# Optimization experiments

Hardware: AMD Instinct MI355X
Metric: run time of the kernel (lower is better)

The kernel has to match this reference:

```python
import jax, jax.numpy as jnp
import numpy as np

TOP_K = 2


def setup_inputs() -> dict:
    key = jax.random.key(0)
    k1, k2, k3, k4, k5 = jax.random.split(key, 5)
    T, H, I, E = 1024, 1024, 2816, 8
    return {
        "hidden_states": jax.random.normal(k1, (T, H), dtype=jnp.float32),
        "router_logits": jax.random.normal(k2, (T, E), dtype=jnp.float32),
        "w1": jax.random.normal(k3, (E, I, H), dtype=jnp.float32) * 0.02,
        "w3": jax.random.normal(k4, (E, I, H), dtype=jnp.float32) * 0.02,
        "w2": jax.random.normal(k5, (E, H, I), dtype=jnp.float32) * 0.02,
    }


def _gate_weights(router_logits):
    # top-k softmax with renormalization (Mixtral-style routing)
    probs = jax.nn.softmax(router_logits, axis=-1)          # [T, E]
    vals, idx = jax.lax.top_k(probs, TOP_K)                  # [T, K]
    vals = vals / jnp.sum(vals, axis=-1, keepdims=True)
    E = router_logits.shape[-1]
    # dense per-expert gate [T, E]: scatter top-k weights via one-hot
    onehot = jax.nn.one_hot(idx, E, dtype=vals.dtype)        # [T, K, E]
    return jnp.einsum("tk,tke->te", vals, onehot)


def reference(hidden_states, router_logits, w1, w3, w2):
    x = hidden_states.reshape(-1, hidden_states.shape[-1])   # [T, H]
    gate = _gate_weights(router_logits)                      # [T, E]
    # GatedMLP per expert: silu(x @ w1^T) * (x @ w3^T) @ w2^T
    h1 = jnp.einsum("th,eih->tei", x, w1)                    # [T, E, I]
    h3 = jnp.einsum("th,eih->tei", x, w3)
    act = jax.nn.silu(h1) * h3                               # [T, E, I]
    y = jnp.einsum("tei,ehi->teh", act, w2)                  # [T, E, H]
    out = jnp.einsum("teh,te->th", y, gate)                  # weighted combine
    return out
```

## Files before the change

kernel.cpp:

```cpp
#include <hip/hip_runtime.h>
#include <stdint.h>

#define T_TOK 1024
#define H_DIM 1024
#define I_DIM 2816
#define E_NUM 8

typedef __attribute__((ext_vector_type(8))) short bf16x8;
typedef __attribute__((ext_vector_type(4))) float f32x4;

struct Meta { int counts[E_NUM]; int tiles[E_NUM]; int offs[E_NUM]; };

__device__ __forceinline__ unsigned short f2b(float f) {
    unsigned u = __float_as_uint(f);
    u += 0x7fffu + ((u >> 16) & 1u);
    return (unsigned short)(u >> 16);
}

__global__ void route_kernel(const float* __restrict__ logits,
                             int* __restrict__ tok, float* __restrict__ gate,
                             Meta* __restrict__ meta) {
    __shared__ int cnt[E_NUM];
    const int tid = threadIdx.x;
    if (tid < E_NUM) cnt[tid] = 0;
    for (int j = tid; j < E_NUM * T_TOK; j += 1024) { tok[j] = 0; gate[j] = 0.f; }
    __syncthreads();

    float p[E_NUM];
    const float* lrow = logits + tid * E_NUM;
    float m = -1e30f;
    #pragma unroll
    for (int e = 0; e < E_NUM; ++e) { p[e] = lrow[e]; m = fmaxf(m, p[e]); }
    #pragma unroll
    for (int e = 0; e < E_NUM; ++e) p[e] = __expf(p[e] - m);
    int e0 = 0; float v0 = p[0];
    #pragma unroll
    for (int e = 1; e < E_NUM; ++e) if (p[e] > v0) { v0 = p[e]; e0 = e; }
    int e1 = -1; float v1 = -1.f;
    #pragma unroll
    for (int e = 0; e < E_NUM; ++e) if (e != e0 && p[e] > v1) { v1 = p[e]; e1 = e; }
    const float inv = 1.f / (v0 + v1);
    const float g0 = v0 * inv, g1 = v1 * inv;

    const int p0 = atomicAdd(&cnt[e0], 1);
    const int p1 = atomicAdd(&cnt[e1], 1);
    tok[e0 * T_TOK + p0] = tid; gate[e0 * T_TOK + p0] = g0;
    tok[e1 * T_TOK + p1] = tid; gate[e1 * T_TOK + p1] = g1;
    __syncthreads();
    if (tid == 0) {
        int off = 0;
        for (int e = 0; e < E_NUM; ++e) {
            const int c = cnt[e];
            const int t = (c + 127) >> 7;
            meta->counts[e] = c; meta->tiles[e] = t; meta->offs[e] = off;
            off += t * 128;
        }
    }
}

__global__ void cvt_x_kernel(const float* __restrict__ x, unsigned short* __restrict__ xb) {
    const int i = blockIdx.x * blockDim.x + threadIdx.x;
    const float4 v = ((const float4*)x)[i];
    ushort4 o; o.x = f2b(v.x); o.y = f2b(v.y); o.z = f2b(v.z); o.w = f2b(v.w);
    ((ushort4*)xb)[i] = o;
}

__launch_bounds__(256)
__global__ void gemm1_kernel(const unsigned short* __restrict__ xb,
                             const float* __restrict__ w1,
                             const float* __restrict__ w3,
                             const int* __restrict__ tok,
                             const Meta* __restrict__ meta,
                             unsigned short* __restrict__ act) {
    const int e = blockIdx.y;
    const int mt = blockIdx.z;
    if (mt >= meta->tiles[e]) return;
    const int it = blockIdx.x;
    const int tid = threadIdx.x;

    __shared__ __align__(16) unsigned short As[128 * 32];
    __shared__ __align__(16) unsigned short B1s[64 * 32];
    __shared__ __align__(16) unsigned short B3s[64 * 32];

    const int arow = tid >> 2, asub = tid & 3;
    const int t0 = tok[e * T_TOK + mt * 128 + arow];
    const int t1 = tok[e * T_TOK + mt * 128 + 64 + arow];
    const unsigned short* ap0 = xb + (size_t)t0 * H_DIM + asub * 8;
    const unsigned short* ap1 = xb + (size_t)t1 * H_DIM + asub * 8;
    unsigned short* al0 = &As[arow * 32 + asub * 8];
    unsigned short* al1 = &As[(64 + arow) * 32 + asub * 8];

    const int brow = tid >> 3, bsub = tid & 7;
    const size_t wbase = (size_t)e * I_DIM * H_DIM + (size_t)(it * 64) * H_DIM;
    const float* b1p0 = w1 + wbase + (size_t)brow * H_DIM + bsub * 4;
    const float* b1p1 = w1 + wbase + (size_t)(32 + brow) * H_DIM + bsub * 4;
    const float* b3p0 = w3 + wbase + (size_t)brow * H_DIM + bsub * 4;
    const float* b3p1 = w3 + wbase + (size_t)(32 + brow) * H_DIM + bsub * 4;
    unsigned short* bl10 = &B1s[brow * 32 + bsub * 4];
    unsigned short* bl11 = &B1s[(32 + brow) * 32 + bsub * 4];
    unsigned short* bl30 = &B3s[brow * 32 + bsub * 4];
    unsigned short* bl31 = &B3s[(32 + brow) * 32 + bsub * 4];

    const int wave = tid >> 6, lane = tid & 63;
    const int quad = lane >> 4, l15 = lane & 15;
    const int mbase = (wave >> 1) * 64;
    const int nbase = (wave & 1) * 32;

    f32x4 acc1[4][2], acc3[4][2];
    #pragma unroll
    for (int mi = 0; mi < 4; ++mi)
        #pragma unroll
        for (int ni = 0; ni < 2; ++ni) {
            acc1[mi][ni] = (f32x4){0.f, 0.f, 0.f, 0.f};
            acc3[mi][ni] = (f32x4){0.f, 0.f, 0.f, 0.f};
        }

    uint4 ra0 = *(const uint4*)(ap0), ra1 = *(const uint4*)(ap1);
    float4 r10 = *(const float4*)(b1p0), r11 = *(const float4*)(b1p1);
    float4 r30 = *(const float4*)(b3p0), r31 = *(const float4*)(b3p1);

    const int NK = H_DIM / 32;
    for (int ks = 0; ks < NK; ++ks) {
        __syncthreads();
        *(uint4*)al0 = ra0;
        *(uint4*)al1 = ra1;
        ushort4 c;
        c.x = f2b(r10.x); c.y = f2b(r10.y); c.z = f2b(r10.z); c.w = f2b(r10.w); *(ushort4*)bl10 = c;
        c.x = f2b(r11.x); c.y = f2b(r11.y); c.z = f2b(r11.z); c.w = f2b(r11.w); *(ushort4*)bl11 = c;
        c.x = f2b(r30.x); c.y = f2b(r30.y); c.z = f2b(r30.z); c.w = f2b(r30.w); *(ushort4*)bl30 = c;
        c.x = f2b(r31.x); c.y = f2b(r31.y); c.z = f2b(r31.z); c.w = f2b(r31.w); *(ushort4*)bl31 = c;
        __syncthreads();
        if (ks + 1 < NK) {
            const int k0 = (ks + 1) * 32;
            ra0 = *(const uint4*)(ap0 + k0);  ra1 = *(const uint4*)(ap1 + k0);
            r10 = *(const float4*)(b1p0 + k0); r11 = *(const float4*)(b1p1 + k0);
            r30 = *(const float4*)(b3p0 + k0); r31 = *(const float4*)(b3p1 + k0);
        }
        bf16x8 a[4];
        #pragma unroll
        for (int mi = 0; mi < 4; ++mi)
            a[mi] = *(const bf16x8*)&As[(mbase + mi * 16 + l15) * 32 + quad * 8];
        bf16x8 b1f[2], b3f[2];
        #pragma unroll
        for (int ni = 0; ni < 2; ++ni) {
            b1f[ni] = *(const bf16x8*)&B1s[(nbase + ni * 16 + l15) * 32 + quad * 8];
            b3f[ni] = *(const bf16x8*)&B3s[(nbase + ni * 16 + l15) * 32 + quad * 8];
        }
        #pragma unroll
        for (int mi = 0; mi < 4; ++mi)
            #pragma unroll
            for (int ni = 0; ni < 2; ++ni) {
                acc1[mi][ni] = __builtin_amdgcn_mfma_f32_16x16x32_bf16(a[mi], b1f[ni], acc1[mi][ni], 0, 0, 0);
                acc3[mi][ni] = __builtin_amdgcn_mfma_f32_16x16x32_bf16(a[mi], b3f[ni], acc3[mi][ni], 0, 0, 0);
            }
    }

    const int opad = meta->offs[e];
    #pragma unroll
    for (int mi = 0; mi < 4; ++mi)
        #pragma unroll
        for (int ni = 0; ni < 2; ++ni)
            #pragma unroll
            for (int rr = 0; rr < 4; ++rr) {
                const float v1 = acc1[mi][ni][rr];
                const float v3 = acc3[mi][ni][rr];
                const float s = v1 / (1.f + __expf(-v1)) * v3;
                const int row = opad + mt * 128 + mbase + mi * 16 + quad * 4 + rr;
                const int col = it * 64 + nbase + ni * 16 + l15;
                act[(size_t)row * I_DIM + col] = f2b(s);
            }
}

__launch_bounds__(256)
__global__ void gemm2_kernel(const unsigned short* __restrict__ act,
                             const float* __restrict__ w2,
                             const int* __restrict__ tok,
                             const float* __restrict__ gate,
                             const Meta* __restrict__ meta,
                             float* __restrict__ out) {
    const int e = blockIdx.y;
    const int mt = blockIdx.z;
    if (mt >= meta->tiles[e]) return;
    const int it = blockIdx.x;
    const int tid = threadIdx.x;
    const int opad = meta->offs[e];

    __shared__ __align__(16) unsigned short As[128 * 32];
    __shared__ __align__(16) unsigned short Bs[64 * 32];

    const int arow = tid >> 2, asub = tid & 3;
    const unsigned short* ap0 = act + (size_t)(opad + mt * 128 + arow) * I_DIM + asub * 8;
    const unsigned short* ap1 = act + (size_t)(opad + mt * 128 + 64 + arow) * I_DIM + asub * 8;
    unsigned short* al0 = &As[arow * 32 + asub * 8];
    unsigned short* al1 = &As[(64 + arow) * 32 + asub * 8];

    const int brow = tid >> 3, bsub = tid & 7;
    const size_t wbase = (size_t)e * H_DIM * I_DIM + (size_t)(it * 64) * I_DIM;
    const float* bp0 = w2 + wbase + (size_t)brow * I_DIM + bsub * 4;
    const float* bp1 = w2 + wbase + (size_t)(32 + brow) * I_DIM + bsub * 4;
    unsigned short* bl0 = &Bs[brow * 32 + bsub * 4];
    unsigned short* bl1 = &Bs[(32 + brow) * 32 + bsub * 4];

    const int wave = tid >> 6, lane = tid & 63;
    const int quad = lane >> 4, l15 = lane & 15;
    const int mbase = (wave >> 1) * 64;
    const int nbase = (wave & 1) * 32;

    f32x4 acc[4][2];
    #pragma unroll
    for (int mi = 0; mi < 4; ++mi)
        #pragma unroll
        for (int ni = 0; ni < 2; ++ni) acc[mi][ni] = (f32x4){0.f, 0.f, 0.f, 0.f};

    uint4 ra0 = *(const uint4*)(ap0), ra1 = *(const uint4*)(ap1);
    float4 rb0 = *(const float4*)(bp0), rb1 = *(const float4*)(bp1);

    const int NK = I_DIM / 32;
    for (int ks = 0; ks < NK; ++ks) {
        __syncthreads();
        *(uint4*)al0 = ra0;
        *(uint4*)al1 = ra1;
        ushort4 c;
        c.x = f2b(rb0.x); c.y = f2b(rb0.y); c.z = f2b(rb0.z); c.w = f2b(rb0.w); *(ushort4*)bl0 = c;
        c.x = f2b(rb1.x); c.y = f2b(rb1.y); c.z = f2b(rb1.z); c.w = f2b(rb1.w); *(ushort4*)bl1 = c;
        __syncthreads();
        if (ks + 1 < NK) {
            const int k0 = (ks + 1) * 32;
            ra0 = *(const uint4*)(ap0 + k0); ra1 = *(const uint4*)(ap1 + k0);
            rb0 = *(const float4*)(bp0 + k0); rb1 = *(const float4*)(bp1 + k0);
        }
        bf16x8 a[4];
        #pragma unroll
        for (int mi = 0; mi < 4; ++mi)
            a[mi] = *(const bf16x8*)&As[(mbase + mi * 16 + l15) * 32 + quad * 8];
        bf16x8 bf[2];
        #pragma unroll
        for (int ni = 0; ni < 2; ++ni)
            bf[ni] = *(const bf16x8*)&Bs[(nbase + ni * 16 + l15) * 32 + quad * 8];
        #pragma unroll
        for (int mi = 0; mi < 4; ++mi)
            #pragma unroll
            for (int ni = 0; ni < 2; ++ni)
                acc[mi][ni] = __builtin_amdgcn_mfma_f32_16x16x32_bf16(a[mi], bf[ni], acc[mi][ni], 0, 0, 0);
    }

    #pragma unroll
    for (int mi = 0; mi < 4; ++mi)
        #pragma unroll
        for (int rr = 0; rr < 4; ++rr) {
            const int r = mt * 128 + mbase + mi * 16 + quad * 4 + rr;
            const int t = tok[e * T_TOK + r];
            const float g = gate[e * T_TOK + r];
            #pragma unroll
            for (int ni = 0; ni < 2; ++ni) {
                const int col = it * 64 + nbase + ni * 16 + l15;
                atomicAdd(&out[(size_t)t * H_DIM + col], g * acc[mi][ni][rr]);
            }
        }
}

extern "C" void kernel_launch(void* const* d_in, const int* in_sizes, int n_in,
                              void* d_out, int out_size, void* d_ws, size_t ws_size,
                              hipStream_t stream) {
    const float* x      = (const float*)d_in[0];
    const float* logits = (const float*)d_in[1];
    const float* w1     = (const float*)d_in[2];
    const float* w3     = (const float*)d_in[3];
    const float* w2     = (const float*)d_in[4];
    float* out = (float*)d_out;

    char* ws = (char*)d_ws;
    int*   tok  = (int*)ws;
    float* gate = (float*)(ws + 32768);
    Meta*  meta = (Meta*)(ws + 65536);
    unsigned short* xb  = (unsigned short*)(ws + 131072);
    unsigned short* act = (unsigned short*)(ws + 131072 + 2097152);

    hipMemsetAsync(d_out, 0, (size_t)T_TOK * H_DIM * sizeof(float), stream);
    route_kernel<<<1, 1024, 0, stream>>>(logits, tok, gate, meta);
    cvt_x_kernel<<<T_TOK * H_DIM / 4 / 256, 256, 0, stream>>>(x, xb);
    gemm1_kernel<<<dim3(I_DIM / 64, E_NUM, 8), 256, 0, stream>>>(xb, w1, w3, tok, meta, act);
    gemm2_kernel<<<dim3(H_DIM / 64, E_NUM, 8), 256, 0, stream>>>(act, w2, tok, gate, meta, out);
}
```

Baseline: 392.1 us.

## Widen K tile to 64, use 512-thread blocks, swizzle LDS, split-K gemm2

Both GEMMs now use 512-thread blocks with eight waves, each owning a 32x32 sub-tile. The K step per iteration doubles to 64 and shared memory is XOR-swizzled to avoid bank conflicts. gemm2 splits its I dimension four ways to raise block count and parallelism, relying on the existing atomic accumulation. It also skips atomics for zero-gate padded rows. The costs are four times as many atomic adds on the output and less register-level reuse per wave.

```diff
diff --git a/kernel.cpp b/kernel.cpp
--- a/kernel.cpp
+++ b/kernel.cpp
@@ -5,6 +5,8 @@
 #define H_DIM 1024
 #define I_DIM 2816
 #define E_NUM 8
+#define KSPLIT 4
+#define K2_STEPS (I_DIM / 64 / KSPLIT)
 
 typedef __attribute__((ext_vector_type(8))) short bf16x8;
 typedef __attribute__((ext_vector_type(4))) float f32x4;
@@ -15,6 +17,13 @@
     unsigned u = __float_as_uint(f);
     u += 0x7fffu + ((u >> 16) & 1u);
     return (unsigned short)(u >> 16);
+}
+
+__device__ __forceinline__ uint4 pack8(const float4 a, const float4 b) {
+    union { unsigned short us[8]; uint4 v; } u;
+    u.us[0] = f2b(a.x); u.us[1] = f2b(a.y); u.us[2] = f2b(a.z); u.us[3] = f2b(a.w);
+    u.us[4] = f2b(b.x); u.us[5] = f2b(b.y); u.us[6] = f2b(b.z); u.us[7] = f2b(b.w);
+    return u.v;
 }
 
 __global__ void route_kernel(const float* __restrict__ logits,
@@ -65,7 +74,7 @@
     ((ushort4*)xb)[i] = o;
 }
 
-__launch_bounds__(256)
+__launch_bounds__(512)
 __global__ void gemm1_kernel(const unsigned short* __restrict__ xb,
                              const float* __restrict__ w1,
                              const float* __restrict__ w3,
@@ -78,100 +87,103 @@
     const int it = blockIdx.x;
     const int tid = threadIdx.x;
 
-    __shared__ __align__(16) unsigned short As[128 * 32];
-    __shared__ __align__(16) unsigned short B1s[64 * 32];
-    __shared__ __align__(16) unsigned short B3s[64 * 32];
-
-    const int arow = tid >> 2, asub = tid & 3;
-    const int t0 = tok[e * T_TOK + mt * 128 + arow];
-    const int t1 = tok[e * T_TOK + mt * 128 + 64 + arow];
-    const unsigned short* ap0 = xb + (size_t)t0 * H_DIM + asub * 8;
-    const unsigned short* ap1 = xb + (size_t)t1 * H_DIM + asub * 8;
-    unsigned short* al0 = &As[arow * 32 + asub * 8];
-    unsigned short* al1 = &As[(64 + arow) * 32 + asub * 8];
-
-    const int brow = tid >> 3, bsub = tid & 7;
-    const size_t wbase = (size_t)e * I_DIM * H_DIM + (size_t)(it * 64) * H_DIM;
-    const float* b1p0 = w1 + wbase + (size_t)brow * H_DIM + bsub * 4;
-    const float* b1p1 = w1 + wbase + (size_t)(32 + brow) * H_DIM + bsub * 4;
-    const float* b3p0 = w3 + wbase + (size_t)brow * H_DIM + bsub * 4;
-    const float* b3p1 = w3 + wbase + (size_t)(32 + brow) * H_DIM + bsub * 4;
-    unsigned short* bl10 = &B1s[brow * 32 + bsub * 4];
-    unsigned short* bl11 = &B1s[(32 + brow) * 32 + bsub * 4];
-    unsigned short* bl30 = &B3s[brow * 32 + bsub * 4];
-    unsigned short* bl31 = &B3s[(32 + brow) * 32 + bsub * 4];
+    __shared__ __align__(16) unsigned short As[128 * 64];
+    __shared__ __align__(16) unsigned short B1s[64 * 64];
+    __shared__ __align__(16) unsigned short B3s[64 * 64];
+
+    const int srow = tid >> 3, ssub = tid & 7;
+    const int t0 = tok[e * T_TOK + mt * 128 + srow];
+    const int t1 = tok[e * T_TOK + mt * 128 + 64 + srow];
+    const unsigned short* ap0 = xb + (size_t)t0 * H_DIM + ssub * 8;
+    const unsigned short* ap1 = xb + (size_t)t1 * H_DIM + ssub * 8;
+    const int scol = (ssub * 8) ^ ((srow & 7) << 3);
+    unsigned short* al0 = &As[srow * 64 + scol];
+    unsigned short* al1 = &As[(64 + srow) * 64 + scol];
+
+    const size_t wbase = (size_t)e * I_DIM * H_DIM + (size_t)(it * 64 + srow) * H_DIM + ssub * 8;
+    const float* b1p = w1 + wbase;
+    const float* b3p = w3 + wbase;
+    unsigned short* bl1 = &B1s[srow * 64 + scol];
+    unsigned short* bl3 = &B3s[srow * 64 + scol];
 
     const int wave = tid >> 6, lane = tid & 63;
     const int quad = lane >> 4, l15 = lane & 15;
-    const int mbase = (wave >> 1) * 64;
+    const int mbase = (wave >> 1) * 32;
     const int nbase = (wave & 1) * 32;
 
-    f32x4 acc1[4][2], acc3[4][2];
-    #pragma unroll
-    for (int mi = 0; mi < 4; ++mi)
-        #pragma unroll
-        for (int ni = 0; ni < 2; ++ni) {
-            acc1[mi][ni] = (f32x4){0.f, 0.f, 0.f, 0.f};
-            acc3[mi][ni] = (f32x4){0.f, 0.f, 0.f, 0.f};
-        }
-
-    uint4 ra0 = *(const uint4*)(ap0), ra1 = *(const uint4*)(ap1);
-    float4 r10 = *(const float4*)(b1p0), r11 = *(const float4*)(b1p1);
-    float4 r30 = *(const float4*)(b3p0), r31 = *(const float4*)(b3p1);
-
-    const int NK = H_DIM / 32;
+    f32x4 acc1[2][2], acc3[2][2];
+    #pragma unroll
+    for (int m = 0; m < 2; ++m)
+        #pragma unroll
+        for (int n = 0; n < 2; ++n) {
+            acc1[m][n] = (f32x4){0.f, 0.f, 0.f, 0.f};
+            acc3[m][n] = (f32x4){0.f, 0.f, 0.f, 0.f};
+        }
+
+    uint4 ra0 = *(const uint4*)ap0, ra1 = *(const uint4*)ap1;
+    float4 rb1a = *(const float4*)b1p, rb1b = *(const float4*)(b1p + 4);
+    float4 rb3a = *(const float4*)b3p, rb3b = *(const float4*)(b3p + 4);
+
+    const int NK = H_DIM / 64;
     for (int ks = 0; ks < NK; ++ks) {
         __syncthreads();
         *(uint4*)al0 = ra0;
         *(uint4*)al1 = ra1;
-        ushort4 c;
-        c.x = f2b(r10.x); c.y = f2b(r10.y); c.z = f2b(r10.z); c.w = f2b(r10.w); *(ushort4*)bl10 = c;
-        c.x = f2b(r11.x); c.y = f2b(r11.y); c.z = f2b(r11.z); c.w = f2b(r11.w); *(ushort4*)bl11 = c;
-        c.x = f2b(r30.x); c.y = f2b(r30.y); c.z = f2b(r30.z); c.w = f2b(r30.w); *(ushort4*)bl30 = c;
-        c.x = f2b(r31.x); c.y = f2b(r31.y); c.z = f2b(r31.z); c.w = f2b(r31.w); *(ushort4*)bl31 = c;
+        *(uint4*)bl1 = pack8(rb1a, rb1b);
+        *(uint4*)bl3 = pack8(rb3a, rb3b);
         __syncthreads();
         if (ks + 1 < NK) {
-            const int k0 = (ks + 1) * 32;
+            const int k0 = (ks + 1) * 64;
             ra0 = *(const uint4*)(ap0 + k0);  ra1 = *(const uint4*)(ap1 + k0);
-            r10 = *(const float4*)(b1p0 + k0); r11 = *(const float4*)(b1p1 + k0);
-            r30 = *(const float4*)(b3p0 + k0); r31 = *(const float4*)(b3p1 + k0);
-        }
-        bf16x8 a[4];
-        #pragma unroll
-        for (int mi = 0; mi < 4; ++mi)
-            a[mi] = *(const bf16x8*)&As[(mbase + mi * 16 + l15) * 32 + quad * 8];
-        bf16x8 b1f[2], b3f[2];
-        #pragma unroll
-        for (int ni = 0; ni < 2; ++ni) {
-            b1f[ni] = *(const bf16x8*)&B1s[(nbase + ni * 16 + l15) * 32 + quad * 8];
-            b3f[ni] = *(const bf16x8*)&B3s[(nbase + ni * 16 + l15) * 32 + quad * 8];
-        }
-        #pragma unroll
-        for (int mi = 0; mi < 4; ++mi)
-            #pragma unroll
-            for (int ni = 0; ni < 2; ++ni) {
-                acc1[mi][ni] = __builtin_amdgcn_mfma_f32_16x16x32_bf16(a[mi], b1f[ni], acc1[mi][ni], 0, 0, 0);
-                acc3[mi][ni] = __builtin_amdgcn_mfma_f32_16x16x32_bf16(a[mi], b3f[ni], acc3[mi][ni], 0, 0, 0);
+            rb1a = *(const float4*)(b1p + k0); rb1b = *(const float4*)(b1p + k0 + 4);
+            rb3a = *(const float4*)(b3p + k0); rb3b = *(const float4*)(b3p + k0 + 4);
+        }
+        bf16x8 a[2][2], bf1[2][2], bf3[2][2];
+        #pragma unroll
+        for (int m = 0; m < 2; ++m) {
+            const int row = mbase + m * 16 + l15;
+            #pragma unroll
+            for (int kk = 0; kk < 2; ++kk)
+                a[m][kk] = *(const bf16x8*)&As[row * 64 + ((kk * 32 + quad * 8) ^ ((row & 7) << 3))];
+        }
+        #pragma unroll
+        for (int n = 0; n < 2; ++n) {
+            const int row = nbase + n * 16 + l15;
+            #pragma unroll
+            for (int kk = 0; kk < 2; ++kk) {
+                const int off = row * 64 + ((kk * 32 + quad * 8) ^ ((row & 7) << 3));
+                bf1[n][kk] = *(const bf16x8*)&B1s[off];
+                bf3[n][kk] = *(const bf16x8*)&B3s[off];
             }
+        }
+        #pragma unroll
+        for (int m = 0; m < 2; ++m)
+            #pragma unroll
+            for (int n = 0; n < 2; ++n)
+                #pragma unroll
+                for (int kk = 0; kk < 2; ++kk) {
+                    acc1[m][n] = __builtin_amdgcn_mfma_f32_16x16x32_bf16(a[m][kk], bf1[n][kk], acc1[m][n], 0, 0, 0);
+                    acc3[m][n] = __builtin_amdgcn_mfma_f32_16x16x32_bf16(a[m][kk], bf3[n][kk], acc3[m][n], 0, 0, 0);
+                }
     }
 
     const int opad = meta->offs[e];
     #pragma unroll
-    for (int mi = 0; mi < 4; ++mi)
-        #pragma unroll
-        for (int ni = 0; ni < 2; ++ni)
+    for (int m = 0; m < 2; ++m)
+        #pragma unroll
+        for (int n = 0; n < 2; ++n)
             #pragma unroll
             for (int rr = 0; rr < 4; ++rr) {
-                const float v1 = acc1[mi][ni][rr];
-                const float v3 = acc3[mi][ni][rr];
+                const float v1 = acc1[m][n][rr];
+                const float v3 = acc3[m][n][rr];
                 const float s = v1 / (1.f + __expf(-v1)) * v3;
-                const int row = opad + mt * 128 + mbase + mi * 16 + quad * 4 + rr;
-                const int col = it * 64 + nbase + ni * 16 + l15;
+                const int row = opad + mt * 128 + mbase + m * 16 + quad * 4 + rr;
+                const int col = it * 64 + nbase + n * 16 + l15;
                 act[(size_t)row * I_DIM + col] = f2b(s);
             }
 }
 
-__launch_bounds__(256)
+__launch_bounds__(512)
 __global__ void gemm2_kernel(const unsigned short* __restrict__ act,
                              const float* __restrict__ w2,
                              const int* __restrict__ tok,
@@ -179,82 +191,89 @@
                              const Meta* __restrict__ meta,
                              float* __restrict__ out) {
     const int e = blockIdx.y;
-    const int mt = blockIdx.z;
+    const int mt = blockIdx.z >> 2;
+    const int kb = blockIdx.z & 3;
     if (mt >= meta->tiles[e]) return;
     const int it = blockIdx.x;
     const int tid = threadIdx.x;
     const int opad = meta->offs[e];
 
-    __shared__ __align__(16) unsigned short As[128 * 32];
-    __shared__ __align__(16) unsigned short Bs[64 * 32];
-
-    const int arow = tid >> 2, asub = tid & 3;
-    const unsigned short* ap0 = act + (size_t)(opad + mt * 128 + arow) * I_DIM + asub * 8;
-    const unsigned short* ap1 = act + (size_t)(opad + mt * 128 + 64 + arow) * I_DIM + asub * 8;
-    unsigned short* al0 = &As[arow * 32 + asub * 8];
-    unsigned short* al1 = &As[(64 + arow) * 32 + asub * 8];
-
-    const int brow = tid >> 3, bsub = tid & 7;
-    const size_t wbase = (size_t)e * H_DIM * I_DIM + (size_t)(it * 64) * I_DIM;
-    const float* bp0 = w2 + wbase + (size_t)brow * I_DIM + bsub * 4;
-    const float* bp1 = w2 + wbase + (size_t)(32 + brow) * I_DIM + bsub * 4;
-    unsigned short* bl0 = &Bs[brow * 32 + bsub * 4];
-    unsigned short* bl1 = &Bs[(32 + brow) * 32 + bsub * 4];
+    __shared__ __align__(16) unsigned short As[128 * 64];
+    __shared__ __align__(16) unsigned short Bs[64 * 64];
+
+    const int srow = tid >> 3, ssub = tid & 7;
+    const int kbase = kb * (K2_STEPS * 64);
+    const unsigned short* ap0 = act + (size_t)(opad + mt * 128 + srow) * I_DIM + kbase + ssub * 8;
+    const unsigned short* ap1 = ap0 + (size_t)64 * I_DIM;
+    const int scol = (ssub * 8) ^ ((srow & 7) << 3);
+    unsigned short* al0 = &As[srow * 64 + scol];
+    unsigned short* al1 = &As[(64 + srow) * 64 + scol];
+
+    const float* bp = w2 + (size_t)e * H_DIM * I_DIM + (size_t)(it * 64 + srow) * I_DIM + kbase + ssub * 8;
+    unsigned short* bl = &Bs[srow * 64 + scol];
 
     const int wave = tid >> 6, lane = tid & 63;
     const int quad = lane >> 4, l15 = lane & 15;
-    const int mbase = (wave >> 1) * 64;
+    const int mbase = (wave >> 1) * 32;
     const int nbase = (wave & 1) * 32;
 
-    f32x4 acc[4][2];
-    #pragma unroll
-    for (int mi = 0; mi < 4; ++mi)
-        #pragma unroll
-        for (int ni = 0; ni < 2; ++ni) acc[mi][ni] = (f32x4){0.f, 0.f, 0.f, 0.f};
-
-    uint4 ra0 = *(const uint4*)(ap0), ra1 = *(const uint4*)(ap1);
-    float4 rb0 = *(const float4*)(bp0), rb1 = *(const float4*)(bp1);
-
-    const int NK = I_DIM / 32;
-    for (int ks = 0; ks < NK; ++ks) {
+    f32x4 acc[2][2];
+    #pragma unroll
+    for (int m = 0; m < 2; ++m)
+        #pragma unroll
+        for (int n = 0; n < 2; ++n) acc[m][n] = (f32x4){0.f, 0.f, 0.f, 0.f};
+
+    uint4 ra0 = *(const uint4*)ap0, ra1 = *(const uint4*)ap1;
+    float4 rba = *(const float4*)bp, rbb = *(const float4*)(bp + 4);
+
+    for (int ks = 0; ks < K2_STEPS; ++ks) {
         __syncthreads();
         *(uint4*)al0 = ra0;
         *(uint4*)al1 = ra1;
-        ushort4 c;
-        c.x = f2b(rb0.x); c.y = f2b(rb0.y); c.z = f2b(rb0.z); c.w = f2b(rb0.w); *(ushort4*)bl0 = c;
-        c.x = f2b(rb1.x); c.y = f2b(rb1.y); c.z = f2b(rb1.z); c.w = f2b(rb1.w); *(ushort4*)bl1 = c;
+        *(uint4*)bl = pack8(rba, rbb);
         __syncthreads();
-        if (ks + 1 < NK) {
-            const int k0 = (ks + 1) * 32;
+        if (ks + 1 < K2_STEPS) {
+            const int k0 = (ks + 1) * 64;
             ra0 = *(const uint4*)(ap0 + k0); ra1 = *(const uint4*)(ap1 + k0);
-            rb0 = *(const float4*)(bp0 + k0); rb1 = *(const float4*)(bp1 + k0);
-        }
-        bf16x8 a[4];
-        #pragma unroll
-        for (int mi = 0; mi < 4; ++mi)
-            a[mi] = *(const bf16x8*)&As[(mbase + mi * 16 + l15) * 32 + quad * 8];
-        bf16x8 bf[2];
-        #pragma unroll
-        for (int ni = 0; ni < 2; ++ni)
-            bf[ni] = *(const bf16x8*)&Bs[(nbase + ni * 16 + l15) * 32 + quad * 8];
-        #pragma unroll
-        for (int mi = 0; mi < 4; ++mi)
-            #pragma unroll
-            for (int ni = 0; ni < 2; ++ni)
-                acc[mi][ni] = __builtin_amdgcn_mfma_f32_16x16x32_bf16(a[mi], bf[ni], acc[mi][ni], 0, 0, 0);
+            rba = *(const float4*)(bp + k0); rbb = *(const float4*)(bp + k0 + 4);
+        }
+        bf16x8 a[2][2], bf[2][2];
+        #pragma unroll
+        for (int m = 0; m < 2; ++m) {
+            const int row = mbase + m * 16 + l15;
+            #pragma unroll
+            for (int kk = 0; kk < 2; ++kk)
+                a[m][kk] = *(const bf16x8*)&As[row * 64 + ((kk * 32 + quad * 8) ^ ((row & 7) << 3))];
+        }
+        #pragma unroll
+        for (int n = 0; n < 2; ++n) {
+            const int row = nbase + n * 16 + l15;
+            #pragma unroll
+            for (int kk = 0; kk < 2; ++kk)
+                bf[n][kk] = *(const bf16x8*)&Bs[row * 64 + ((kk * 32 + quad * 8) ^ ((row & 7) << 3))];
+        }
+        #pragma unroll
+        for (int m = 0; m < 2; ++m)
+            #pragma unroll
+            for (int n = 0; n < 2; ++n)
+                #pragma unroll
+                for (int kk = 0; kk < 2; ++kk)
+                    acc[m][n] = __builtin_amdgcn_mfma_f32_16x16x32_bf16(a[m][kk], bf[n][kk], acc[m][n], 0, 0, 0);
     }
 
     #pragma unroll
-    for (int mi = 0; mi < 4; ++mi)
+    for (int m = 0; m < 2; ++m)
         #pragma unroll
         for (int rr = 0; rr < 4; ++rr) {
-            const int r = mt * 128 + mbase + mi * 16 + quad * 4 + rr;
+            const int r = mt * 128 + mbase + m * 16 + quad * 4 + rr;
             const int t = tok[e * T_TOK + r];
             const float g = gate[e * T_TOK + r];
-            #pragma unroll
-            for (int ni = 0; ni < 2; ++ni) {
-                const int col = it * 64 + nbase + ni * 16 + l15;
-                atomicAdd(&out[(size_t)t * H_DIM + col], g * acc[mi][ni][rr]);
+            if (g != 0.f) {
+                #pragma unroll
+                for (int n = 0; n < 2; ++n) {
+                    const int col = it * 64 + nbase + n * 16 + l15;
+                    atomicAdd(&out[(size_t)t * H_DIM + col], g * acc[m][n][rr]);
+                }
             }
         }
 }
@@ -279,6 +298,6 @@
     hipMemsetAsync(d_out, 0, (size_t)T_TOK * H_DIM * sizeof(float), stream);
     route_kernel<<<1, 1024, 0, stream>>>(logits, tok, gate, meta);
     cvt_x_kernel<<<T_TOK * H_DIM / 4 / 256, 256, 0, stream>>>(x, xb);
-    gemm1_kernel<<<dim3(I_DIM / 64, E_NUM, 8), 256, 0, stream>>>(xb, w1, w3, tok, meta, act);
-    gemm2_kernel<<<dim3(H_DIM / 64, E_NUM, 8), 256, 0, stream>>>(act, w2, tok, gate, meta, out);
-}
+    gemm1_kernel<<<dim3(I_DIM / 64, E_NUM, 8), 512, 0, stream>>>(xb, w1, w3, tok, meta, act);
+    gemm2_kernel<<<dim3(H_DIM / 64, E_NUM, 8 * KSPLIT), 512, 0, stream>>>(act, w2, tok, gate, meta, out);
+}
```

After: 339.2 us. 13.5% less time.
